# Optimization experiments

Measured on AMD Instinct MI355X. Metric: run time of the kernel, lower is better.

The kernel has to match this reference:

```python
import jax, jax.numpy as jnp
import numpy as np

IN_DIM, HID, N_EXP, TOP_K = 4096, 512, 128, 2
SMOOTH = 0.1
SPARSITY = 0.5

def _gelu(x):
    return jax.nn.gelu(x, approximate=False)  # torch nn.GELU default (erf)


def setup_inputs() -> dict:
    key = jax.random.key(0)
    ks = jax.random.split(key, 24)
    def lin(k, fan_in, shape):
        bound = 1.0 / np.sqrt(fan_in)
        return jax.random.uniform(k, shape, jnp.float32, -bound, bound)
    x = jax.random.normal(ks[0], (4, 2048, IN_DIM), jnp.float32)
    # weights stored as (in, out); apply with x @ W + b
    w_in_proj = lin(ks[1], IN_DIM, (IN_DIM, HID)); b_in_proj = lin(ks[2], IN_DIM, (HID,))
    w_ff1 = lin(ks[3], 2 * HID, (2 * HID, HID)); b_ff1 = lin(ks[4], 2 * HID, (HID,))
    w_ff2 = lin(ks[5], HID, (HID, HID)); b_ff2 = lin(ks[6], HID, (HID,))
    w_ta = lin(ks[7], HID, (HID, HID)); b_ta = lin(ks[8], HID, (HID,))
    w_tb = lin(ks[9], HID, (HID, HID)); b_tb = lin(ks[10], HID, (HID,))
    w_iw = lin(ks[11], HID, (HID, HID)); b_iw = lin(ks[12], HID, (HID,))
    input_b = jnp.zeros((HID,), jnp.float32)
    mask = (jax.random.uniform(ks[13], (HID, HID)) > SPARSITY).astype(jnp.float32)
    w_rw = lin(ks[14], HID, (HID, HID)) * mask  # structured sparsity on recurrent weight
    r_b = jnp.zeros((HID,), jnp.float32)
    w_g1 = lin(ks[15], HID, (HID, 2 * HID)); b_g1 = lin(ks[16], HID, (2 * HID,))
    w_g2 = lin(ks[17], 2 * HID, (2 * HID, N_EXP)); b_g2 = lin(ks[18], 2 * HID, (N_EXP,))
    return dict(x=x, w_in_proj=w_in_proj, b_in_proj=b_in_proj, w_ff1=w_ff1, b_ff1=b_ff1,
                w_ff2=w_ff2, b_ff2=b_ff2, w_ta=w_ta, b_ta=b_ta, w_tb=w_tb, b_tb=b_tb,
                w_iw=w_iw, b_iw=b_iw, input_b=input_b, w_rw=w_rw, r_b=r_b,
                w_g1=w_g1, b_g1=b_g1, w_g2=w_g2, b_g2=b_g2)


def reference(x, w_in_proj, b_in_proj, w_ff1, b_ff1, w_ff2, b_ff2, w_ta, b_ta,
              w_tb, b_tb, w_iw, b_iw, input_b, w_rw, r_b, w_g1, b_g1, w_g2, b_g2):
    B, S, _ = x.shape
    ts = 1.0

    def step(carry, x_t):
        h, prev_probs, first = carry
        xt = x_t @ w_in_proj + b_in_proj                       # (B, HID)
        # CfC cell
        x_cat = jnp.concatenate([xt, h], axis=-1)
        ff1 = _gelu(x_cat @ w_ff1 + b_ff1)
        ff2 = _gelu(ff1 @ w_ff2 + b_ff2)
        t_a = ff2 @ w_ta + b_ta
        t_b = ff2 @ w_tb + b_tb
        t_interp = jax.nn.sigmoid(t_a * ts + t_b)
        inp_c = _gelu(xt @ w_iw + b_iw + input_b)
        rec_c = _gelu(h @ w_rw + r_b)
        new_h = h * (1.0 - t_interp) + t_interp * (inp_c + rec_c)
        # expert gate
        g = _gelu(new_h @ w_g1 + b_g1)
        probs = jax.nn.softmax(g @ w_g2 + b_g2, axis=-1)       # (B, N_EXP)
        probs = jnp.where(first, probs,
                          (1.0 - SMOOTH) * probs + SMOOTH * prev_probs)
        new_prev = jax.lax.stop_gradient(probs)                # .detach() in torch
        top_p, top_i = jax.lax.top_k(probs, TOP_K)
        top_w = top_p / jnp.sum(top_p, axis=-1, keepdims=True)
        return (new_h, new_prev, jnp.array(False)), (top_i, top_w)

    h0 = jnp.zeros((B, HID), x.dtype)
    p0 = jnp.zeros((B, N_EXP), x.dtype)
    carry0 = (h0, p0, jnp.array(True))
    _, (idx, wts) = jax.lax.scan(step, carry0, jnp.swapaxes(x, 0, 1))
    expert_indices = jnp.swapaxes(idx, 0, 1)   # (B, S, TOP_K)
    expert_weights = jnp.swapaxes(wts, 0, 1)   # (B, S, TOP_K)
    return expert_indices, expert_weights
```

## Files before the change

kernel.cpp:

```cpp
#include <hip/hip_runtime.h>
#include <cmath>

#define HID 512
#define NEXP 128
#define BB 4
#define SS 2048
#define NROW (BB*SS)
#define SCAN_BLOCKS 128

typedef unsigned long long u64;
typedef unsigned int u32;

__device__ __forceinline__ float gelu_f(float x){
  return 0.5f*x*(1.0f + erff(x*0.70710678118654752440f));
}

__device__ __forceinline__ u64 aload64(const u64* p){
  return __hip_atomic_load(p, __ATOMIC_RELAXED, __HIP_MEMORY_SCOPE_AGENT);
}
__device__ __forceinline__ void astore64(u64* p, u64 v){
  __hip_atomic_store(p, v, __ATOMIC_RELAXED, __HIP_MEMORY_SCOPE_AGENT);
}
__device__ __forceinline__ u64 packtag(float f, u32 tag){
  return ((u64)__float_as_uint(f) << 32) | (u64)tag;
}

__device__ __forceinline__ void poll2(const u64* exbuf, u32 tag, float* stg, int tid){
  const u64* p0 = exbuf + tid;
  const u64* p1 = exbuf + tid + 256;
  u64 v0 = aload64(p0);
  u64 v1 = aload64(p1);
  while ((u32)v0 != tag) v0 = aload64(p0);
  while ((u32)v1 != tag) v1 = aload64(p1);
  stg[tid]       = __uint_as_float((u32)(v0 >> 32));
  stg[tid + 256] = __uint_as_float((u32)(v1 >> 32));
}

__global__ __launch_bounds__(256) void biwc_k(const float* __restrict__ b_iw,
                                              const float* __restrict__ input_b,
                                              float* __restrict__ biwc)
{
  int i = blockIdx.x*256 + threadIdx.x;
  if (i < HID) biwc[i] = b_iw[i] + input_b[i];
}

template<bool GELU>
__global__ __launch_bounds__(256) void gemm_k(
    const float* __restrict__ A, const float* __restrict__ W,
    const float* __restrict__ bias, float* __restrict__ C,
    int M, int N, int K)
{
  __shared__ float As[16][68];
  __shared__ float Ws[16][68];
  const int tid = threadIdx.x;
  const int mb = blockIdx.y*64, nb = blockIdx.x*64;
  const int tx = tid & 15, ty = tid >> 4;
  const int am = tid >> 2, ak = (tid & 3)*4;
  const int wk = tid >> 4, wn = (tid & 15)*4;
  float acc[4][4] = {};
  const float* Aptr = A + (size_t)(mb+am)*K + ak;
  for (int kt = 0; kt < K; kt += 16){
    float4 av = *(const float4*)(Aptr + kt);
    float4 wv = *(const float4*)(W + (size_t)(kt+wk)*N + nb + wn);
    As[ak  ][am] = av.x; As[ak+1][am] = av.y; As[ak+2][am] = av.z; As[ak+3][am] = av.w;
    *(float4*)&Ws[wk][wn] = wv;
    __syncthreads();
#pragma unroll
    for (int kk = 0; kk < 16; kk++){
      float4 a4 = *(const float4*)&As[kk][ty*4];
      float4 w4 = *(const float4*)&Ws[kk][tx*4];
      float ar[4] = {a4.x, a4.y, a4.z, a4.w};
      float wr[4] = {w4.x, w4.y, w4.z, w4.w};
#pragma unroll
      for (int i = 0; i < 4; i++)
#pragma unroll
        for (int j = 0; j < 4; j++)
          acc[i][j] = fmaf(ar[i], wr[j], acc[i][j]);
    }
    __syncthreads();
  }
#pragma unroll
  for (int i = 0; i < 4; i++){
    int row = mb + ty*4 + i;
    float o[4];
#pragma unroll
    for (int j = 0; j < 4; j++){
      float v = acc[i][j] + bias[nb + tx*4 + j];
      o[j] = GELU ? gelu_f(v) : v;
    }
    float4 o4 = {o[0], o[1], o[2], o[3]};
    *(float4*)(C + (size_t)row*N + nb + tx*4) = o4;
  }
}

__global__ __launch_bounds__(256, 1) void scan_k(
    const float* __restrict__ w_ff1, const float* __restrict__ w_rw,
    const float* __restrict__ w_ff2,
    const float* __restrict__ w_ta, const float* __restrict__ w_tb,
    const float* __restrict__ bff2, const float* __restrict__ b_ta,
    const float* __restrict__ b_tb, const float* __restrict__ rb,
    const float* __restrict__ PRE, const float* __restrict__ INPC,
    float* __restrict__ Hout,
    u64* __restrict__ exh, u64* __restrict__ exf1, u64* __restrict__ exf2)
{
  __shared__ float Wa2[512*32];
  __shared__ float Wb2[512*16];
  __shared__ float Wc2[512*16];
  __shared__ float stg[512];
  __shared__ float red[128];
  __shared__ float rec_loc[16];

  const int tid = threadIdx.x;
  const int b = blockIdx.x >> 5, sub = blockIdx.x & 31;
  const int col0 = sub*16;
  u64* exh_b  = exh  + b*512;
  u64* exf1_b = exf1 + b*512;
  u64* exf2_b = exf2 + b*512;

  for (int idx = tid; idx < 512*32; idx += 256){
    int k = idx >> 5, c = idx & 31;
    float v = (c < 16) ? w_ff1[(size_t)(512+k)*HID + col0 + c]
                       : w_rw[(size_t)k*HID + col0 + (c-16)];
    Wa2[((k>>1)<<6) + (c<<1) + (k&1)] = v;
  }
  for (int idx = tid; idx < 512*16; idx += 256){
    int k = idx >> 4, c = idx & 15;
    Wb2[((k>>1)<<5) + (c<<1) + (k&1)] = w_ff2[(size_t)k*HID + col0 + c];
    Wc2[((k>>1)<<5) + (c<<1) + (k&1)] = w_ta[(size_t)k*HID + col0 + c]
                                      + w_tb[(size_t)k*HID + col0 + c];
  }
  float b3v = 0.f, bff2v = 0.f, rbv = 0.f, h_reg = 0.f;
  if (tid < 16){ b3v = b_ta[col0+tid] + b_tb[col0+tid]; bff2v = bff2[col0+tid]; }
  if (tid >= 16 && tid < 32) rbv = rb[col0 + tid - 16];
  __syncthreads();

  const int cA = tid & 31, pA = tid >> 5;
  const int cB = tid & 15, pB = tid >> 4;

  for (int t = 0; t < SS; t++){
    float pre_v = 0.f, ic_v = 0.f;
    if (tid < 16){
      pre_v = PRE [((size_t)b*SS + t)*HID + col0 + tid];
      ic_v  = INPC[((size_t)b*SS + t)*HID + col0 + tid];
    }
    poll2(exh_b, (u32)t, stg, tid);
    __syncthreads();
    {
      const float2* wp = (const float2*)(Wa2) + (pA<<5) + cA;
      const float2* hp = (const float2*)(stg) + pA;
      float a0=0.f, a1=0.f, a2=0.f, a3=0.f;
#pragma unroll
      for (int j = 0; j < 32; j += 2){
        float2 w0 = wp[(j+0)*256], h0 = hp[(j+0)*8];
        float2 w1 = wp[(j+1)*256], h1 = hp[(j+1)*8];
        a0 = fmaf(w0.x, h0.x, a0); a1 = fmaf(w0.y, h0.y, a1);
        a2 = fmaf(w1.x, h1.x, a2); a3 = fmaf(w1.y, h1.y, a3);
      }
      float acc = (a0+a1)+(a2+a3);
      acc += __shfl_xor(acc, 32);
      if ((tid & 32) == 0) red[(tid>>6)*32 + cA] = acc;
    }
    __syncthreads();
    if (tid < 32){
      float s = red[tid] + red[32+tid] + red[64+tid] + red[96+tid];
      if (tid < 16){
        float v = gelu_f(pre_v + s);
        astore64(&exf1_b[col0 + tid], packtag(v, (u32)(t+1)));
      } else {
        rec_loc[tid-16] = gelu_f(s + rbv);
      }
    }
    poll2(exf1_b, (u32)(t+1), stg, tid);
    __syncthreads();
    {
      const float2* wp = (const float2*)(Wb2) + (pB<<4) + cB;
      const float2* hp = (const float2*)(stg) + pB;
      float a0=0.f, a1=0.f, a2=0.f, a3=0.f;
#pragma unroll
      for (int j = 0; j < 16; j += 2){
        float2 w0 = wp[(j+0)*256], h0 = hp[(j+0)*16];
        float2 w1 = wp[(j+1)*256], h1 = hp[(j+1)*16];
        a0 = fmaf(w0.x, h0.x, a0); a1 = fmaf(w0.y, h0.y, a1);
        a2 = fmaf(w1.x, h1.x, a2); a3 = fmaf(w1.y, h1.y, a3);
      }
      float acc = (a0+a1)+(a2+a3);
      acc += __shfl_xor(acc, 16);
      acc += __shfl_xor(acc, 32);
      if ((tid & 48) == 0) red[(tid>>6)*16 + cB] = acc;
    }
    __syncthreads();
    if (tid < 16){
      float s = red[tid] + red[16+tid] + red[32+tid] + red[48+tid];
      float v = gelu_f(s + bff2v);
      astore64(&exf2_b[col0 + tid], packtag(v, (u32)(t+1)));
    }
    poll2(exf2_b, (u32)(t+1), stg, tid);
    __syncthreads();
    {
      const float2* wp = (const float2*)(Wc2) + (pB<<4) + cB;
      const float2* hp = (const float2*)(stg) + pB;
      float a0=0.f, a1=0.f, a2=0.f, a3=0.f;
#pragma unroll
      for (int j = 0; j < 16; j += 2){
        float2 w0 = wp[(j+0)*256], h0 = hp[(j+0)*16];
        float2 w1 = wp[(j+1)*256], h1 = hp[(j+1)*16];
        a0 = fmaf(w0.x, h0.x, a0); a1 = fmaf(w0.y, h0.y, a1);
        a2 = fmaf(w1.x, h1.x, a2); a3 = fmaf(w1.y, h1.y, a3);
      }
      float acc = (a0+a1)+(a2+a3);
      acc += __shfl_xor(acc, 16);
      acc += __shfl_xor(acc, 32);
      if ((tid & 48) == 0) red[(tid>>6)*16 + cB] = acc;
    }
    __syncthreads();
    if (tid < 16){
      float s = red[tid] + red[16+tid] + red[32+tid] + red[48+tid];
      float ti = 1.0f / (1.0f + expf(-(s + b3v)));
      float nh = h_reg*(1.0f - ti) + ti*(ic_v + rec_loc[tid]);
      h_reg = nh;
      astore64(&exh_b[col0 + tid], packtag(nh, (u32)(t+1)));
      Hout[((size_t)b*SS + t)*HID + col0 + tid] = nh;
    }
  }
}

__global__ __launch_bounds__(256) void softmax_k(const float* __restrict__ LOGITS,
                                                 float* __restrict__ SM)
{
  int wv = threadIdx.x >> 6, lane = threadIdx.x & 63;
  int row = blockIdx.x*4 + wv;
  const float* xp = LOGITS + (size_t)row*NEXP;
  float x0 = xp[lane], x1 = xp[lane+64];
  float m = fmaxf(x0, x1);
#pragma unroll
  for (int d = 1; d < 64; d <<= 1) m = fmaxf(m, __shfl_xor(m, d));
  float e0 = expf(x0 - m), e1 = expf(x1 - m);
  float s = e0 + e1;
#pragma unroll
  for (int d = 1; d < 64; d <<= 1) s += __shfl_xor(s, d);
  float inv = 1.0f / s;
  float* op = SM + (size_t)row*NEXP;
  op[lane] = e0*inv; op[lane+64] = e1*inv;
}

__global__ __launch_bounds__(256) void smooth_topk_k(const float* __restrict__ SM,
                                                     float* __restrict__ out)
{
  int wv = threadIdx.x >> 6, lane = threadIdx.x & 63;
  int row = blockIdx.x*4 + wv;
  int b = row >> 11, t = row & 2047;
  const float* base = SM + (size_t)row*NEXP;
  float a0 = 0.f, a1 = 0.f;
  float coef = 0.9f;
  int nt = t < 20 ? t : 20;
  for (int j = 0; j < nt; j++){
    const float* pj = base - j*NEXP;
    a0 += coef * pj[lane];
    a1 += coef * pj[lane+64];
    coef *= 0.1f;
  }
  if (t < 20){
    const float* s0 = SM + (size_t)b*SS*NEXP;
    float c0 = coef * (1.0f/0.9f);
    a0 += c0 * s0[lane];
    a1 += c0 * s0[lane+64];
  }
  float v0, v1; int i0, i1;
  if (a0 >= a1){ v0=a0; i0=lane;    v1=a1; i1=lane+64; }
  else         { v0=a1; i0=lane+64; v1=a0; i1=lane;    }
#pragma unroll
  for (int d = 1; d < 64; d <<= 1){
    float ov0 = __shfl_xor(v0, d), ov1 = __shfl_xor(v1, d);
    int   oi0 = __shfl_xor(i0, d), oi1 = __shfl_xor(i1, d);
    bool firstMine = (v0 > ov0) || (v0 == ov0 && i0 < oi0);
    float nv0, nv1; int ni0, ni1;
    if (firstMine){
      nv0 = v0; ni0 = i0;
      bool s = (v1 > ov0) || (v1 == ov0 && i1 < oi0);
      nv1 = s ? v1 : ov0; ni1 = s ? i1 : oi0;
    } else {
      nv0 = ov0; ni0 = oi0;
      bool s = (ov1 > v0) || (ov1 == v0 && oi1 < i0);
      nv1 = s ? ov1 : v0; ni1 = s ? oi1 : i0;
    }
    v0 = nv0; v1 = nv1; i0 = ni0; i1 = ni1;
  }
  if (lane == 0){
    float ssum = v0 + v1;
    size_t o = (size_t)row*2;
    out[o]     = (float)i0;
    out[o+1]   = (float)i1;
    out[16384 + o]   = v0 / ssum;
    out[16384 + o+1] = v1 / ssum;
  }
}

extern "C" void kernel_launch(void* const* d_in, const int* in_sizes, int n_in,
                              void* d_out, int out_size, void* d_ws, size_t ws_size,
                              hipStream_t stream)
{
  (void)in_sizes; (void)n_in; (void)out_size;
  const float* x       = (const float*)d_in[0];
  const float* w_in    = (const float*)d_in[1];
  const float* b_in    = (const float*)d_in[2];
  const float* w_ff1   = (const float*)d_in[3];
  const float* b_ff1   = (const float*)d_in[4];
  const float* w_ff2   = (const float*)d_in[5];
  const float* b_ff2   = (const float*)d_in[6];
  const float* w_ta    = (const float*)d_in[7];
  const float* b_ta    = (const float*)d_in[8];
  const float* w_tb    = (const float*)d_in[9];
  const float* b_tb    = (const float*)d_in[10];
  const float* w_iw    = (const float*)d_in[11];
  const float* b_iw    = (const float*)d_in[12];
  const float* input_b = (const float*)d_in[13];
  const float* w_rw    = (const float*)d_in[14];
  const float* r_b     = (const float*)d_in[15];
  const float* w_g1    = (const float*)d_in[16];
  const float* b_g1    = (const float*)d_in[17];
  const float* w_g2    = (const float*)d_in[18];
  const float* b_g2    = (const float*)d_in[19];

  float* ws    = (float*)d_ws;
  float* XT    = ws + 0;
  float* PRE   = ws + 4194304;
  float* INPC  = ws + 8388608;
  float* Hbuf  = ws + 12582912;
  float* G1    = ws + 0;
  float* LOGB  = ws + 8388608;
  float* SM    = ws + 9437184;
  float* biwc  = ws + 16777216;
  u64*   exh   = (u64*)(ws + 16777728);
  u64*   exf1  = (u64*)(ws + 16781824);
  u64*   exf2  = (u64*)(ws + 16785920);
  if (ws_size < (size_t)16790016 * sizeof(float)) return;

  hipMemsetAsync(ws + 16777728, 0, 3 * 2048 * sizeof(u64), stream);

  biwc_k<<<2, 256, 0, stream>>>(b_iw, input_b, biwc);
  gemm_k<false><<<dim3(8, 128), 256, 0, stream>>>(x, w_in, b_in, XT, NROW, 512, 4096);
  gemm_k<false><<<dim3(8, 128), 256, 0, stream>>>(XT, w_ff1, b_ff1, PRE, NROW, 512, 512);
  gemm_k<true ><<<dim3(8, 128), 256, 0, stream>>>(XT, w_iw, biwc, INPC, NROW, 512, 512);
  scan_k<<<SCAN_BLOCKS, 256, 0, stream>>>(w_ff1, w_rw, w_ff2, w_ta, w_tb,
                                          b_ff2, b_ta, b_tb, r_b,
                                          PRE, INPC, Hbuf, exh, exf1, exf2);
  gemm_k<true ><<<dim3(16, 128), 256, 0, stream>>>(Hbuf, w_g1, b_g1, G1, NROW, 1024, 512);
  gemm_k<false><<<dim3(2, 128), 256, 0, stream>>>(G1, w_g2, b_g2, LOGB, NROW, 128, 1024);
  softmax_k<<<2048, 256, 0, stream>>>(LOGB, SM);
  smooth_topk_k<<<2048, 256, 0, stream>>>(SM, (float*)d_out);
}
```

Measured before the change: 10.96 ms.

## Add fast-path non-coherent polling buffers with sticky fallback to agent-scope atomics

The scan's cross-block exchange gains a second set of buffers. These are written with plain global stores and polled with sc0 loads for a bounded number of iterations, and the code falls back permanently to the agent-scope atomic buffers after repeated misses. Blocks are remapped so the batch index is blockIdx&7, with 256 blocks launched and half exiting immediately. The likely intent is to place each batch's 32 blocks on the same XCD so the fast loads can hit a shared L2 instead of going to device-coherent memory. This depends on the hardware's round-robin block-to-XCD assignment, adds extra stores on every step, and needs poison resets at the end.

```diff
diff --git a/kernel.cpp b/kernel.cpp
--- a/kernel.cpp
+++ b/kernel.cpp
@@ -6,7 +6,8 @@
 #define BB 4
 #define SS 2048
 #define NROW (BB*SS)
-#define SCAN_BLOCKS 128
+#define FAST_ITERS 96
+#define FAIL_STICKY 12
 
 typedef unsigned long long u64;
 typedef unsigned int u32;
@@ -21,17 +22,37 @@
 __device__ __forceinline__ void astore64(u64* p, u64 v){
   __hip_atomic_store(p, v, __ATOMIC_RELAXED, __HIP_MEMORY_SCOPE_AGENT);
 }
+__device__ __forceinline__ void fstore64(u64* p, u64 v){
+  asm volatile("global_store_dwordx2 %0, %1, off" :: "v"(p), "v"(v) : "memory");
+}
 __device__ __forceinline__ u64 packtag(float f, u32 tag){
   return ((u64)__float_as_uint(f) << 32) | (u64)tag;
 }
 
-__device__ __forceinline__ void poll2(const u64* exbuf, u32 tag, float* stg, int tid){
-  const u64* p0 = exbuf + tid;
-  const u64* p1 = exbuf + tid + 256;
-  u64 v0 = aload64(p0);
-  u64 v1 = aload64(p1);
-  while ((u32)v0 != tag) v0 = aload64(p0);
-  while ((u32)v1 != tag) v1 = aload64(p1);
+__device__ __forceinline__ void poll2x(const u64* fb, const u64* mb, u32 tag,
+                                       float* stg, int tid,
+                                       int& fails, bool& use_agent){
+  u64 v0 = 0, v1 = 0;
+  bool ok0 = false, ok1 = false;
+  if (!use_agent){
+    const u64* p0 = fb + tid;
+    const u64* p1 = fb + tid + 256;
+    for (int it = 0; it < FAST_ITERS; ++it){
+      u64 a, b;
+      asm volatile("global_load_dwordx2 %0, %2, off sc0\n\t"
+                   "global_load_dwordx2 %1, %3, off sc0\n\t"
+                   "s_waitcnt vmcnt(0)"
+                   : "=&v"(a), "=&v"(b) : "v"(p0), "v"(p1) : "memory");
+      if (!ok0 && (u32)a == tag){ ok0 = true; v0 = a; }
+      if (!ok1 && (u32)b == tag){ ok1 = true; v1 = b; }
+      if (ok0 && ok1) break;
+    }
+    if (!(ok0 && ok1)){
+      if (++fails >= FAIL_STICKY) use_agent = true;
+    }
+  }
+  if (!ok0){ const u64* q = mb + tid;       u64 a; do { a = aload64(q); } while ((u32)a != tag); v0 = a; }
+  if (!ok1){ const u64* q = mb + tid + 256; u64 a; do { a = aload64(q); } while ((u32)a != tag); v1 = a; }
   stg[tid]       = __uint_as_float((u32)(v0 >> 32));
   stg[tid + 256] = __uint_as_float((u32)(v1 >> 32));
 }
@@ -101,7 +122,8 @@
     const float* __restrict__ b_tb, const float* __restrict__ rb,
     const float* __restrict__ PRE, const float* __restrict__ INPC,
     float* __restrict__ Hout,
-    u64* __restrict__ exh, u64* __restrict__ exf1, u64* __restrict__ exf2)
+    u64* __restrict__ exh, u64* __restrict__ exf1, u64* __restrict__ exf2,
+    u64* __restrict__ fexh, u64* __restrict__ fexf1, u64* __restrict__ fexf2)
 {
   __shared__ float Wa2[512*32];
   __shared__ float Wb2[512*16];
@@ -111,11 +133,18 @@
   __shared__ float rec_loc[16];
 
   const int tid = threadIdx.x;
-  const int b = blockIdx.x >> 5, sub = blockIdx.x & 31;
+  const int b = blockIdx.x & 7;
+  if (b >= BB) return;
+  const int sub = blockIdx.x >> 3;
   const int col0 = sub*16;
-  u64* exh_b  = exh  + b*512;
-  u64* exf1_b = exf1 + b*512;
-  u64* exf2_b = exf2 + b*512;
+  u64* exh_b   = exh   + b*512;
+  u64* exf1_b  = exf1  + b*512;
+  u64* exf2_b  = exf2  + b*512;
+  u64* fexh_b  = fexh  + b*512;
+  u64* fexf1_b = fexf1 + b*512;
+  u64* fexf2_b = fexf2 + b*512;
+
+  if (tid < 16) fstore64(&fexh_b[col0 + tid], packtag(0.f, 0u));
 
   for (int idx = tid; idx < 512*32; idx += 256){
     int k = idx >> 5, c = idx & 31;
@@ -136,6 +165,7 @@
 
   const int cA = tid & 31, pA = tid >> 5;
   const int cB = tid & 15, pB = tid >> 4;
+  int fails = 0; bool use_agent = false;
 
   for (int t = 0; t < SS; t++){
     float pre_v = 0.f, ic_v = 0.f;
@@ -143,7 +173,7 @@
       pre_v = PRE [((size_t)b*SS + t)*HID + col0 + tid];
       ic_v  = INPC[((size_t)b*SS + t)*HID + col0 + tid];
     }
-    poll2(exh_b, (u32)t, stg, tid);
+    poll2x(fexh_b, exh_b, (u32)t, stg, tid, fails, use_agent);
     __syncthreads();
     {
       const float2* wp = (const float2*)(Wa2) + (pA<<5) + cA;
@@ -165,12 +195,14 @@
       float s = red[tid] + red[32+tid] + red[64+tid] + red[96+tid];
       if (tid < 16){
         float v = gelu_f(pre_v + s);
-        astore64(&exf1_b[col0 + tid], packtag(v, (u32)(t+1)));
+        u64 pk = packtag(v, (u32)(t+1));
+        fstore64(&fexf1_b[col0 + tid], pk);
+        astore64(&exf1_b[col0 + tid], pk);
       } else {
         rec_loc[tid-16] = gelu_f(s + rbv);
       }
     }
-    poll2(exf1_b, (u32)(t+1), stg, tid);
+    poll2x(fexf1_b, exf1_b, (u32)(t+1), stg, tid, fails, use_agent);
     __syncthreads();
     {
       const float2* wp = (const float2*)(Wb2) + (pB<<4) + cB;
@@ -192,9 +224,11 @@
     if (tid < 16){
       float s = red[tid] + red[16+tid] + red[32+tid] + red[48+tid];
       float v = gelu_f(s + bff2v);
-      astore64(&exf2_b[col0 + tid], packtag(v, (u32)(t+1)));
-    }
-    poll2(exf2_b, (u32)(t+1), stg, tid);
+      u64 pk = packtag(v, (u32)(t+1));
+      fstore64(&fexf2_b[col0 + tid], pk);
+      astore64(&exf2_b[col0 + tid], pk);
+    }
+    poll2x(fexf2_b, exf2_b, (u32)(t+1), stg, tid, fails, use_agent);
     __syncthreads();
     {
       const float2* wp = (const float2*)(Wc2) + (pB<<4) + cB;
@@ -218,9 +252,18 @@
       float ti = 1.0f / (1.0f + expf(-(s + b3v)));
       float nh = h_reg*(1.0f - ti) + ti*(ic_v + rec_loc[tid]);
       h_reg = nh;
-      astore64(&exh_b[col0 + tid], packtag(nh, (u32)(t+1)));
+      u64 pk = packtag(nh, (u32)(t+1));
+      fstore64(&fexh_b[col0 + tid], pk);
+      astore64(&exh_b[col0 + tid], pk);
       Hout[((size_t)b*SS + t)*HID + col0 + tid] = nh;
     }
+  }
+
+  __syncthreads();
+  for (int i = tid; i < 512; i += 256){
+    fstore64(&fexh_b[i],  0xFFFFFFFFull);
+    fstore64(&fexf1_b[i], 0xFFFFFFFFull);
+    fstore64(&fexf2_b[i], 0xFFFFFFFFull);
   }
 }
 
@@ -333,7 +376,10 @@
   u64*   exh   = (u64*)(ws + 16777728);
   u64*   exf1  = (u64*)(ws + 16781824);
   u64*   exf2  = (u64*)(ws + 16785920);
-  if (ws_size < (size_t)16790016 * sizeof(float)) return;
+  u64*   fexh  = (u64*)(ws + 16790016);
+  u64*   fexf1 = (u64*)(ws + 16794112);
+  u64*   fexf2 = (u64*)(ws + 16798208);
+  if (ws_size < (size_t)16802304 * sizeof(float)) return;
 
   hipMemsetAsync(ws + 16777728, 0, 3 * 2048 * sizeof(u64), stream);
 
@@ -341,9 +387,10 @@
   gemm_k<false><<<dim3(8, 128), 256, 0, stream>>>(x, w_in, b_in, XT, NROW, 512, 4096);
   gemm_k<false><<<dim3(8, 128), 256, 0, stream>>>(XT, w_ff1, b_ff1, PRE, NROW, 512, 512);
   gemm_k<true ><<<dim3(8, 128), 256, 0, stream>>>(XT, w_iw, biwc, INPC, NROW, 512, 512);
-  scan_k<<<SCAN_BLOCKS, 256, 0, stream>>>(w_ff1, w_rw, w_ff2, w_ta, w_tb,
-                                          b_ff2, b_ta, b_tb, r_b,
-                                          PRE, INPC, Hbuf, exh, exf1, exf2);
+  scan_k<<<256, 256, 0, stream>>>(w_ff1, w_rw, w_ff2, w_ta, w_tb,
+                                  b_ff2, b_ta, b_tb, r_b,
+                                  PRE, INPC, Hbuf, exh, exf1, exf2,
+                                  fexh, fexf1, fexf2);
   gemm_k<true ><<<dim3(16, 128), 256, 0, stream>>>(Hbuf, w_g1, b_g1, G1, NROW, 1024, 512);
   gemm_k<false><<<dim3(2, 128), 256, 0, stream>>>(G1, w_g2, b_g2, LOGB, NROW, 128, 1024);
   softmax_k<<<2048, 256, 0, stream>>>(LOGB, SM);
```

Result: no change. 11.00 ms (+0.4%).
